# Kernel optimization log

Measured on AMD Instinct MI355X. Metric: run time of the kernel, lower is better.

## Reference

```python
import jax, jax.numpy as jnp
import numpy as np

B, S, D = 64, 512, 1024


def setup_inputs() -> dict:
    key = jax.random.key(0)
    k_h, k_w = jax.random.split(key)
    last_hidden_state = jax.random.normal(k_h, (B, S, D), dtype=jnp.float32)
    # word_ids: sorted, contiguous subword->word indices per row (tokenizer word_ids).
    inc = jax.random.bernoulli(k_w, 0.5, (B, S)).astype(jnp.int32)
    inc = inc.at[:, 0].set(0)  # first token starts word 0
    word_ids = jnp.cumsum(inc, axis=1)  # [B, S], max ~ S/2 words
    return {"last_hidden_state": last_hidden_state, "word_ids": word_ids}


def reference(last_hidden_state, word_ids):
    # Faithful, vectorized version of merge_subword_representation:
    # out[i, w] = mean of last_hidden_state[i, t] over t with word_ids[i, t] == w,
    # for w in [0, tot_words_i); remaining positions keep original values.
    b, s, d = last_hidden_state.shape
    seg_sum = jax.vmap(
        lambda h, w: jax.ops.segment_sum(h, w, num_segments=s)
    )(last_hidden_state, word_ids)                                  # [B, S, D]
    cnt = jax.vmap(
        lambda w: jax.ops.segment_sum(jnp.ones((s,), last_hidden_state.dtype), w, num_segments=s)
    )(word_ids)                                                     # [B, S]
    means = seg_sum / jnp.maximum(cnt, 1.0)[..., None]              # safe: valid segments have cnt>=1
    tot_words = jnp.max(word_ids, axis=1) + 1                       # [B]
    pos = jnp.arange(s)
    write_mask = pos[None, :] < tot_words[:, None]                  # [B, S]
    return jnp.where(write_mask[..., None], means, last_hidden_state)
```

## Files before the change

### kernel.cpp

```cpp
#include <hip/hip_runtime.h>

#define BS 64
#define SS 512
#define DD 1024
#define NVEC (DD / 4)

typedef float f4 __attribute__((ext_vector_type(4)));

__global__ __launch_bounds__(512) void bounds_kernel(
    const int* __restrict__ wid,
    unsigned int* __restrict__ bounds)
{
    const int b = blockIdx.x;
    const int t = threadIdx.x;
    const int* row = wid + b * SS;

    __shared__ int s_lo[SS + 1];
    __shared__ int s_tot;

    const int w_t  = row[t];
    const int prev = (t == 0) ? -1 : row[t - 1];
    if (t == SS - 1) { s_tot = w_t + 1; s_lo[w_t + 1] = SS; }
    if (w_t != prev) s_lo[w_t] = t;
    __syncthreads();

    const int tot = s_tot;
    unsigned int val;
    if (t < tot) {
        const int lo  = s_lo[t];
        const int len = s_lo[t + 1] - lo;
        val = (unsigned int)lo | ((unsigned int)len << 16);
    } else {
        val = 0xFFFFFFFFu;
    }
    bounds[b * SS + t] = val;
}

__global__ __launch_bounds__(256) void merge_subword_kernel(
    const float* __restrict__ h,
    const unsigned int* __restrict__ bounds,
    float* __restrict__ out)
{
    const int w = blockIdx.x;
    const int b = blockIdx.y;
    const unsigned int bd = bounds[b * SS + w];
    const int tid = threadIdx.x;

    f4* dst = (f4*)(out + ((size_t)b * SS + w) * DD);

    if (bd == 0xFFFFFFFFu) {
        const f4* src = (const f4*)(h + ((size_t)b * SS + w) * DD);
        __builtin_nontemporal_store(src[tid], dst + tid);
    } else {
        const int lo  = (int)(bd & 0xFFFFu);
        const int len = (int)(bd >> 16);
        const float inv = 1.0f / (float)len;
        f4 acc = (f4)(0.f);
        const f4* base = (const f4*)(h + ((size_t)b * SS + lo) * DD);
        for (int t = 0; t < len; ++t) {
            acc += base[(size_t)t * NVEC + tid];
        }
        acc *= inv;
        __builtin_nontemporal_store(acc, dst + tid);
    }
}

extern "C" void kernel_launch(void* const* d_in, const int* in_sizes, int n_in,
                              void* d_out, int out_size, void* d_ws, size_t ws_size,
                              hipStream_t stream) {
    (void)in_sizes; (void)n_in; (void)out_size; (void)ws_size;
    const float* h   = (const float*)d_in[0];
    const int*   wid = (const int*)d_in[1];
    float*       out = (float*)d_out;
    unsigned int* bounds = (unsigned int*)d_ws;

    bounds_kernel<<<dim3(BS), dim3(SS), 0, stream>>>(wid, bounds);
    merge_subword_kernel<<<dim3(SS, BS), dim3(256), 0, stream>>>(h, bounds, out);
}
```

Before: 56.54 us.

## Assign one wave per output row and unify copy path as length-one segment

Each 64-lane wave now handles four output rows in sequence, and each lane loads four float4 per source token. The merge grid shrinks from 32768 blocks to 2048. Rows past the word count are encoded as segments of length one starting at themselves, so the copy branch disappears and all rows take the same averaging loop. This cuts block launch overhead and adds memory-level parallelism per thread, but gives fewer waves in flight across the device and serialises rows within each wave.

```diff
diff --git a/kernel.cpp b/kernel.cpp
--- a/kernel.cpp
+++ b/kernel.cpp
@@ -3,7 +3,11 @@
 #define BS 64
 #define SS 512
 #define DD 1024
-#define NVEC (DD / 4)
+#define ROWS (BS * SS)
+#define ROWS_PER_WAVE 4
+#define WAVES_PER_BLOCK 4
+#define ROWS_PER_BLOCK (ROWS_PER_WAVE * WAVES_PER_BLOCK)
+#define NBLOCKS (ROWS / ROWS_PER_BLOCK)
 
 typedef float f4 __attribute__((ext_vector_type(4)));
 
@@ -31,7 +35,7 @@
         const int len = s_lo[t + 1] - lo;
         val = (unsigned int)lo | ((unsigned int)len << 16);
     } else {
-        val = 0xFFFFFFFFu;
+        val = (unsigned int)t | (1u << 16);
     }
     bounds[b * SS + t] = val;
 }
@@ -41,27 +45,36 @@
     const unsigned int* __restrict__ bounds,
     float* __restrict__ out)
 {
-    const int w = blockIdx.x;
-    const int b = blockIdx.y;
-    const unsigned int bd = bounds[b * SS + w];
-    const int tid = threadIdx.x;
+    const int wave = (int)threadIdx.x >> 6;
+    const int lane = (int)threadIdx.x & 63;
+    const int row0 = (int)blockIdx.x * ROWS_PER_BLOCK + wave * ROWS_PER_WAVE;
 
-    f4* dst = (f4*)(out + ((size_t)b * SS + w) * DD);
+    const unsigned int bd4 = bounds[row0 + (lane & 3)];
 
-    if (bd == 0xFFFFFFFFu) {
-        const f4* src = (const f4*)(h + ((size_t)b * SS + w) * DD);
-        __builtin_nontemporal_store(src[tid], dst + tid);
-    } else {
+    #pragma unroll
+    for (int k = 0; k < ROWS_PER_WAVE; ++k) {
+        const unsigned int bd = (unsigned int)__builtin_amdgcn_readlane((int)bd4, k);
+        const int r   = row0 + k;
         const int lo  = (int)(bd & 0xFFFFu);
         const int len = (int)(bd >> 16);
         const float inv = 1.0f / (float)len;
-        f4 acc = (f4)(0.f);
-        const f4* base = (const f4*)(h + ((size_t)b * SS + lo) * DD);
+
+        const f4* bp = (const f4*)(h + ((size_t)((r & ~(SS - 1)) + lo) * DD));
+        f4 a0 = (f4)(0.f), a1 = (f4)(0.f), a2 = (f4)(0.f), a3 = (f4)(0.f);
         for (int t = 0; t < len; ++t) {
-            acc += base[(size_t)t * NVEC + tid];
+            const f4* p = bp + (size_t)t * (DD / 4) + lane;
+            a0 += p[0 * 64];
+            a1 += p[1 * 64];
+            a2 += p[2 * 64];
+            a3 += p[3 * 64];
         }
-        acc *= inv;
-        __builtin_nontemporal_store(acc, dst + tid);
+        a0 *= inv; a1 *= inv; a2 *= inv; a3 *= inv;
+
+        f4* dst = (f4*)(out + (size_t)r * DD) + lane;
+        __builtin_nontemporal_store(a0, dst + 0 * 64);
+        __builtin_nontemporal_store(a1, dst + 1 * 64);
+        __builtin_nontemporal_store(a2, dst + 2 * 64);
+        __builtin_nontemporal_store(a3, dst + 3 * 64);
     }
 }
 
@@ -75,5 +88,5 @@
     unsigned int* bounds = (unsigned int*)d_ws;
 
     bounds_kernel<<<dim3(BS), dim3(SS), 0, stream>>>(wid, bounds);
-    merge_subword_kernel<<<dim3(SS, BS), dim3(256), 0, stream>>>(h, bounds, out);
+    merge_subword_kernel<<<dim3(NBLOCKS), dim3(256), 0, stream>>>(h, bounds, out);
 }
```

Result: slower. 61.69 us (+9.1%).

## Restructure merge to token-chunk tasks reading each input row once

Applied to the files above, without the earlier changes.

The merge kernel now splits work by input-token chunks of 8 rather than by output word. Each wave loads 8 input rows into registers and, at the token that starts each word, sums that word's tokens from registers, reading from global memory only for words that extend past the chunk. Tail positions are copied straight from registers. The goal is to read the input tensor about once instead of re-reading rows for both the merge and the tail copy, at the cost of more registers, divergent branches, and dropping the nontemporal stores.

```diff
diff --git a/kernel.cpp b/kernel.cpp
--- a/kernel.cpp
+++ b/kernel.cpp
@@ -3,13 +3,17 @@
 #define BS 64
 #define SS 512
 #define DD 1024
-#define NVEC (DD / 4)
+#define CH 8
+#define NCHUNK (SS / CH)
+#define QPT 4
+#define TASKS (BS * NCHUNK * QPT)
+#define NBLOCKS (TASKS / 4)
 
 typedef float f4 __attribute__((ext_vector_type(4)));
 
-__global__ __launch_bounds__(512) void bounds_kernel(
+__global__ __launch_bounds__(512) void desc_kernel(
     const int* __restrict__ wid,
-    unsigned int* __restrict__ bounds)
+    unsigned int* __restrict__ desc)
 {
     const int b = blockIdx.x;
     const int t = threadIdx.x;
@@ -24,44 +28,61 @@
     if (w_t != prev) s_lo[w_t] = t;
     __syncthreads();
 
-    const int tot = s_tot;
-    unsigned int val;
-    if (t < tot) {
-        const int lo  = s_lo[t];
-        const int len = s_lo[t + 1] - lo;
-        val = (unsigned int)lo | ((unsigned int)len << 16);
-    } else {
-        val = 0xFFFFFFFFu;
+    unsigned int v = 0;
+    if (t >= s_tot) v |= 0x80000000u;
+    if (w_t != prev) {
+        const int len = s_lo[w_t + 1] - t;
+        v |= ((unsigned int)len << 16) | (unsigned int)w_t;
     }
-    bounds[b * SS + t] = val;
+    desc[b * SS + t] = v;
 }
 
 __global__ __launch_bounds__(256) void merge_subword_kernel(
     const float* __restrict__ h,
-    const unsigned int* __restrict__ bounds,
+    const unsigned int* __restrict__ desc,
     float* __restrict__ out)
 {
-    const int w = blockIdx.x;
-    const int b = blockIdx.y;
-    const unsigned int bd = bounds[b * SS + w];
-    const int tid = threadIdx.x;
+    const int wave = (int)threadIdx.x >> 6;
+    const int lane = (int)threadIdx.x & 63;
+    const int task = (int)blockIdx.x * 4 + wave;
 
-    f4* dst = (f4*)(out + ((size_t)b * SS + w) * DD);
+    const int q     = task & 3;
+    const int tmp   = task >> 2;
+    const int chunk = tmp & (NCHUNK - 1);
+    const int b     = tmp >> 6;
+    const int t0    = chunk * CH;
 
-    if (bd == 0xFFFFFFFFu) {
-        const f4* src = (const f4*)(h + ((size_t)b * SS + w) * DD);
-        __builtin_nontemporal_store(src[tid], dst + tid);
-    } else {
-        const int lo  = (int)(bd & 0xFFFFu);
-        const int len = (int)(bd >> 16);
-        const float inv = 1.0f / (float)len;
-        f4 acc = (f4)(0.f);
-        const f4* base = (const f4*)(h + ((size_t)b * SS + lo) * DD);
-        for (int t = 0; t < len; ++t) {
-            acc += base[(size_t)t * NVEC + tid];
+    const f4* hp = (const f4*)h;
+    f4*       op = (f4*)out;
+    const int rowbase = b * SS + t0;
+    const int sl      = q * 64 + lane;
+
+    const unsigned int dvec = desc[rowbase + (lane & 7)];
+
+    f4 p[CH];
+    #pragma unroll
+    for (int i = 0; i < CH; ++i) p[i] = hp[(rowbase + i) * 256 + sl];
+
+    #pragma unroll
+    for (int i = 0; i < CH; ++i) {
+        const unsigned int d =
+            (unsigned int)__builtin_amdgcn_readlane((int)dvec, i);
+        if (d & 0x80000000u) {
+            op[(rowbase + i) * 256 + sl] = p[i];
         }
-        acc *= inv;
-        __builtin_nontemporal_store(acc, dst + tid);
+        const int len = (int)((d >> 16) & 0x7FFFu);
+        if (len) {
+            f4 acc = p[i];
+            #pragma unroll
+            for (int j = 1; j < CH - i; ++j)
+                if (j < len) acc += p[i + j];
+            for (int j = CH - i; j < len; ++j)
+                acc += hp[(rowbase + i + j) * 256 + sl];
+            const float inv = 1.0f / (float)len;
+            acc *= inv;
+            const int w = (int)(d & 0xFFFFu);
+            op[(b * SS + w) * 256 + sl] = acc;
+        }
     }
 }
 
@@ -72,8 +93,8 @@
     const float* h   = (const float*)d_in[0];
     const int*   wid = (const int*)d_in[1];
     float*       out = (float*)d_out;
-    unsigned int* bounds = (unsigned int*)d_ws;
+    unsigned int* desc = (unsigned int*)d_ws;
 
-    bounds_kernel<<<dim3(BS), dim3(SS), 0, stream>>>(wid, bounds);
-    merge_subword_kernel<<<dim3(SS, BS), dim3(256), 0, stream>>>(h, bounds, out);
+    desc_kernel<<<dim3(BS), dim3(SS), 0, stream>>>(wid, desc);
+    merge_subword_kernel<<<dim3(NBLOCKS), dim3(256), 0, stream>>>(h, desc, out);
 }
```

Measured after the change: 53.05 us. 1.07x faster.
